# Kernel optimization log

Measured on AMD Instinct MI355X. Metric: run time of the kernel, lower is better.

## Reference

```python
import jax, jax.numpy as jnp
import numpy as np

B, R, C, H, NB, NH, V = 1, 24, 128, 256, 2, 8, 32
DFF = 4 * H


def _ln(x, g, b):
    m = x.mean(-1, keepdims=True)
    v = x.var(-1, keepdims=True)
    return (x - m) / jnp.sqrt(v + 1e-5) * g + b


def _attn(x, wq, wk, wv, wo):
    # x: [..., S, H]; full (dense) multi-head self-attention over axis -2
    d = H // NH
    lead = x.shape[:-1]
    q = (x @ wq).reshape(*lead, NH, d)
    k = (x @ wk).reshape(*lead, NH, d)
    v = (x @ wv).reshape(*lead, NH, d)
    s = jnp.einsum('...qhd,...khd->...hqk', q, k) / np.float32(np.sqrt(d))
    p = jax.nn.softmax(s, axis=-1)
    o = jnp.einsum('...hqk,...khd->...qhd', p, v)
    return o.reshape(*lead, H) @ wo


def setup_inputs() -> dict:
    key = jax.random.key(0)
    ks = iter(jax.random.split(key, 40))

    def nrm(shape, s=0.02):
        return jax.random.normal(next(ks), shape, jnp.float32) * s

    # pair matrix: C(R,2) rows, each selecting (summing) two sequences
    pairs = np.array([(i, j) for i in range(R) for j in range(i + 1, R)], np.int64)
    P = pairs.shape[0]  # 276
    pm = np.zeros((P, R), np.float32)
    pm[np.arange(P)[:, None], pairs] = 1.0

    inp = {
        'x': jax.random.randint(next(ks), (B, R, C), 0, V, jnp.int32),
        'pm': jnp.asarray(pm),
        'emb': nrm((V, H), 1.0),
        'ln1_g': jnp.ones((NB, H)), 'ln1_b': jnp.zeros((NB, H)),
        'wq_r': nrm((NB, H, H)), 'wk_r': nrm((NB, H, H)),
        'wv_r': nrm((NB, H, H)), 'wo_r': nrm((NB, H, H)),
        'ln2_g': jnp.ones((NB, H)), 'ln2_b': jnp.zeros((NB, H)),
        'wq_c': nrm((NB, H, H)), 'wk_c': nrm((NB, H, H)),
        'wv_c': nrm((NB, H, H)), 'wo_c': nrm((NB, H, H)),
        'ln3_g': jnp.ones((NB, H)), 'ln3_b': jnp.zeros((NB, H)),
        'fw1': nrm((NB, H, DFF)), 'fb1': jnp.zeros((NB, DFF)),
        'fw2': nrm((NB, DFF, H)), 'fb2': jnp.zeros((NB, H)),
        'pw1': nrm((H, DFF)), 'pb1': jnp.zeros((DFF,)),
        'pw2': nrm((DFF, 1)), 'pb2': jnp.zeros((1,)),
        'uw': nrm((C, 1)), 'ub': jnp.zeros((1,)),
    }
    return inp


def reference(x, pm, emb, ln1_g, ln1_b, wq_r, wk_r, wv_r, wo_r,
              ln2_g, ln2_b, wq_c, wk_c, wv_c, wo_c, ln3_g, ln3_b,
              fw1, fb1, fw2, fb2, pw1, pb1, pw2, pb2, uw, ub):
    h = emb[x]                                   # [B,R,C,H]
    # pair_matrix @ x : pairwise gather-add over the row (sequence) axis
    h = jnp.einsum('pr,brch->bpch', pm, h)       # [B,P,C,H]
    for i in range(NB):
        # row attention: along columns C, independent per pair
        h = h + _attn(_ln(h, ln1_g[i], ln1_b[i]), wq_r[i], wk_r[i], wv_r[i], wo_r[i])
        # column attention: along pairs P, independent per column
        hc = jnp.swapaxes(h, 1, 2)               # [B,C,P,H]
        a = _attn(_ln(hc, ln2_g[i], ln2_b[i]), wq_c[i], wk_c[i], wv_c[i], wo_c[i])
        h = h + jnp.swapaxes(a, 1, 2)
        # feed-forward
        z = _ln(h, ln3_g[i], ln3_b[i])
        h = h + (jax.nn.gelu(z @ fw1[i] + fb1[i], approximate=False) @ fw2[i] + fb2[i])
    y = jax.nn.gelu(h @ pw1 + pb1, approximate=False) @ pw2 + pb2  # [B,P,C,1]
    y = y.squeeze(-1)                            # [B,P,C]
    y = (y @ uw + ub).squeeze(-1)                # [B,P]
    return y
```

## Files before the change

### kernel.cpp

```cpp
#include <hip/hip_runtime.h>
#include <math.h>

#define HH    256
#define NHEAD 8
#define HD    32
#define CC    128
#define RR    24
#define PP    276
#define NBLK  2
#define DFF   1024
#define MTOK  (PP*CC)

typedef float          f32x4  __attribute__((ext_vector_type(4)));
typedef short          bf16x8 __attribute__((ext_vector_type(8)));
typedef unsigned int   u32x2  __attribute__((ext_vector_type(2)));
typedef unsigned short u16;

__device__ __forceinline__ float gelu_f(float x) {
    return 0.5f * x * (1.0f + erff(x * 0.7071067811865476f));
}
__device__ __forceinline__ u16 f2b(float f) {
    unsigned u = __builtin_bit_cast(unsigned, f);
    unsigned r = (u + 0x7fffu + ((u >> 16) & 1u)) >> 16;
    return (u16)r;
}
__device__ __forceinline__ float b2f(u16 b) {
    unsigned u = ((unsigned)b) << 16;
    return __builtin_bit_cast(float, u);
}
__device__ __forceinline__ unsigned cvt_pk_bf16(float lo, float hi) {
    unsigned r;
    asm("v_cvt_pk_bf16_f32 %0, %1, %2" : "=v"(r) : "v"(lo), "v"(hi));
    return r;
}
__device__ __forceinline__ void gload16(const void* g, void* l) {
    __builtin_amdgcn_global_load_lds(
        (const __attribute__((address_space(1))) unsigned int*)g,
        (__attribute__((address_space(3))) unsigned int*)l, 16, 0, 0);
}

__global__ __launch_bounds__(256) void k_embed(
    const int* __restrict__ x, const float* __restrict__ pm,
    const float* __restrict__ emb, float* __restrict__ h) {
    const int p = blockIdx.x, c = blockIdx.y, t = threadIdx.x;
    float acc = 0.f;
    for (int r = 0; r < RR; ++r) {
        float w = pm[p * RR + r];
        if (w != 0.f) {
            int tok = x[r * CC + c];
            acc += w * emb[(size_t)tok * HH + t];
        }
    }
    h[((size_t)p * CC + c) * HH + t] = acc;
}

__global__ __launch_bounds__(256) void k_ln(
    const float* __restrict__ in, u16* __restrict__ out,
    const float* __restrict__ g, const float* __restrict__ b) {
    const int lane = threadIdx.x & 63, wid = threadIdx.x >> 6;
    const float4 gv = *(const float4*)&g[lane * 4];
    const float4 bv = *(const float4*)&b[lane * 4];
    #pragma unroll
    for (int rr = 0; rr < 2; ++rr) {
        const int row = blockIdx.x * 8 + wid * 2 + rr;
        const float4 v = *(const float4*)&in[(size_t)row * HH + lane * 4];
        float s  = v.x + v.y + v.z + v.w;
        float s2 = v.x * v.x + v.y * v.y + v.z * v.z + v.w * v.w;
        #pragma unroll
        for (int off = 32; off; off >>= 1) {
            s  += __shfl_xor(s,  off);
            s2 += __shfl_xor(s2, off);
        }
        const float mean = s * (1.f / HH);
        const float rstd = rsqrtf(s2 * (1.f / HH) - mean * mean + 1e-5f);
        const float o0 = (v.x - mean) * rstd * gv.x + bv.x;
        const float o1 = (v.y - mean) * rstd * gv.y + bv.y;
        const float o2 = (v.z - mean) * rstd * gv.z + bv.z;
        const float o3 = (v.w - mean) * rstd * gv.w + bv.w;
        u32x2 o;
        o.x = cvt_pk_bf16(o0, o1);
        o.y = cvt_pk_bf16(o2, o3);
        *(u32x2*)&out[(size_t)row * HH + lane * 4] = o;
    }
}

__global__ __launch_bounds__(256) void k_cvtT(
    const float* __restrict__ src, u16* __restrict__ dst,
    int R, int Cc, int dstStride, float mul) {
    __shared__ float tile[32][33];
    const size_t so = (size_t)blockIdx.z * R * Cc;
    const size_t dOff = (size_t)blockIdx.z * dstStride;
    const int r0 = blockIdx.x * 32, c0 = blockIdx.y * 32;
    const int tx = threadIdx.x & 31, ty = threadIdx.x >> 5;
    #pragma unroll
    for (int i = 0; i < 4; ++i)
        tile[ty + 8 * i][tx] = src[so + (size_t)(r0 + ty + 8 * i) * Cc + c0 + tx];
    __syncthreads();
    #pragma unroll
    for (int i = 0; i < 4; ++i)
        dst[dOff + (size_t)(c0 + ty + 8 * i) * R + r0 + tx] = f2b(mul * tile[tx][ty + 8 * i]);
}

#define BM 128
#define BN 64
#define BK 32
template<bool BIAS, bool GELU, bool RES, bool OF32, bool OBF16>
__global__ __launch_bounds__(256) void k_mgemm(
    const u16* __restrict__ A,
    const u16* __restrict__ Wt,
    const float* __restrict__ bias,
    float* __restrict__ C,
    u16* __restrict__ Cb,
    int M, int N, int K) {
    __shared__ __align__(16) char smem[36864];
    u16 (*Al)[BM * BK] = (u16(*)[BM * BK])smem;
    u16 (*Bl)[BN * BK] = (u16(*)[BN * BK])(smem + 24576);
    const int tid = threadIdx.x;
    const int wid = tid >> 6, lane = tid & 63;
    const int wr = wid >> 1, wc = wid & 1;
    const int l16 = lane & 15, lh = lane >> 4;

    const int nwg = gridDim.x;
    const int ntx = N >> 6;
    const int swz = (blockIdx.x & 7) * (nwg >> 3) + (blockIdx.x >> 3);
    const int row0 = (swz / ntx) * BM, col0 = (swz % ntx) * BN;

    int rA[2], pA[2];
    #pragma unroll
    for (int i = 0; i < 2; ++i) {
        const int d = tid + i * 256;
        rA[i] = d >> 2;
        pA[i] = (d & 3) ^ ((rA[i] >> 1) & 3);
    }
    const int nB = tid >> 2;
    const int pB = (tid & 3) ^ ((nB >> 1) & 3);
    const int nt = K / BK;

    auto stage = [&](int buf, int kt) {
        #pragma unroll
        for (int i = 0; i < 2; ++i)
            gload16(A + (size_t)(row0 + rA[i]) * K + kt + pA[i] * 8,
                    (char*)&Al[buf][0] + (wid * 64 + i * 256) * 16);
        gload16(Wt + (size_t)(col0 + nB) * K + kt + pB * 8,
                (char*)&Bl[buf][0] + (wid * 64) * 16);
    };

    f32x4 acc[4][2];
    #pragma unroll
    for (int m = 0; m < 4; ++m)
        #pragma unroll
        for (int n = 0; n < 2; ++n) acc[m][n] = (f32x4){0.f, 0.f, 0.f, 0.f};

    stage(0, 0);
    stage(1, BK);
    for (int t = 0; t < nt; ++t) {
        const int cur = t % 3;
        if (t + 1 < nt) asm volatile("s_waitcnt vmcnt(3)" ::: "memory");
        else            asm volatile("s_waitcnt vmcnt(0)" ::: "memory");
        __builtin_amdgcn_s_barrier();
        __builtin_amdgcn_sched_barrier(0);
        if (t + 2 < nt) stage((t + 2) % 3, (t + 2) * BK);
        bf16x8 af[4], bfr[2];
        #pragma unroll
        for (int m = 0; m < 4; ++m) {
            const int r = wr * 64 + m * 16 + l16;
            af[m] = *(const bf16x8*)((const char*)&Al[cur][0]
                     + r * 64 + ((lh ^ ((r >> 1) & 3)) << 4));
        }
        #pragma unroll
        for (int n = 0; n < 2; ++n) {
            const int nn = wc * 32 + n * 16 + l16;
            bfr[n] = *(const bf16x8*)((const char*)&Bl[cur][0]
                     + nn * 64 + ((lh ^ ((nn >> 1) & 3)) << 4));
        }
        asm volatile("s_waitcnt lgkmcnt(0)" ::: "memory");
        __builtin_amdgcn_sched_barrier(0);
        __builtin_amdgcn_s_setprio(1);
        #pragma unroll
        for (int m = 0; m < 4; ++m)
            #pragma unroll
            for (int n = 0; n < 2; ++n)
                acc[m][n] = __builtin_amdgcn_mfma_f32_16x16x32_bf16(
                    bfr[n], af[m], acc[m][n], 0, 0, 0);
        __builtin_amdgcn_s_setprio(0);
    }

    __syncthreads();
    char* Ct = smem;
    const int lh4 = lh * 4;
    #pragma unroll
    for (int m = 0; m < 4; ++m) {
        const int r = wr * 64 + m * 16 + l16;
        #pragma unroll
        for (int n = 0; n < 2; ++n) {
            const int c = wc * 32 + n * 16 + lh4;
            const int bo = (r * BN + c) * 4 ^ ((r & 7) << 4);
            *(f32x4*)(Ct + bo) = acc[m][n];
        }
    }
    __syncthreads();
    #pragma unroll
    for (int i = 0; i < 8; ++i) {
        const int chunk = tid + i * 256;
        const int r = chunk >> 4, c4 = (chunk & 15) * 4;
        const int bo = (r * BN + c4) * 4 ^ ((r & 7) << 4);
        f32x4 v = *(const f32x4*)(Ct + bo);
        const int colg = col0 + c4;
        const size_t off = (size_t)(row0 + r) * N + colg;
        if (BIAS) v += *(const f32x4*)&bias[colg];
        if (GELU) {
            v[0] = gelu_f(v[0]); v[1] = gelu_f(v[1]);
            v[2] = gelu_f(v[2]); v[3] = gelu_f(v[3]);
        }
        if (RES) v += *(const f32x4*)&C[off];
        if (OF32) __builtin_nontemporal_store(v, (f32x4*)&C[off]);
        if (OBF16) {
            u32x2 o;
            o.x = cvt_pk_bf16(v[0], v[1]);
            o.y = cvt_pk_bf16(v[2], v[3]);
            __builtin_nontemporal_store(o, (u32x2*)&Cb[off]);
        }
    }
}

template<int NQT>
__global__ __launch_bounds__(384) void k_fattn(
    const u16* __restrict__ qg, const u16* __restrict__ kg,
    const u16* __restrict__ vg, u16* __restrict__ og,
    int S, int base_mul, int stride, int rowH) {
    const int head = blockIdx.y;
    const int base = blockIdx.x * base_mul;
    const int tid  = threadIdx.x;
    const int w = tid >> 6, lane = tid & 63;
    const int l16 = lane & 15, lh = lane >> 4;

    __shared__ u16 Vt[32 * 296];

    const int nkt = (S + 15) >> 4;
    const int nch = (nkt + 1) >> 1;
    const int KP  = nch * 32;

    unsigned* Vw = (unsigned*)Vt;
    for (int it = tid; it < (KP >> 1) * 4; it += blockDim.x) {
        const int kp = it >> 2, d8 = (it & 3) * 8;
        const int k0 = kp * 2, k1 = k0 + 1;
        uint4 a = make_uint4(0u, 0u, 0u, 0u), b = a;
        if (k0 < S) a = *(const uint4*)(vg + (size_t)(base + k0 * stride) * rowH + head * HD + d8);
        if (k1 < S) b = *(const uint4*)(vg + (size_t)(base + k1 * stride) * rowH + head * HD + d8);
        Vw[(d8 + 0) * 148 + kp] = (a.x & 0xffffu) | (b.x << 16);
        Vw[(d8 + 1) * 148 + kp] = (a.x >> 16)     | (b.x & 0xffff0000u);
        Vw[(d8 + 2) * 148 + kp] = (a.y & 0xffffu) | (b.y << 16);
        Vw[(d8 + 3) * 148 + kp] = (a.y >> 16)     | (b.y & 0xffff0000u);
        Vw[(d8 + 4) * 148 + kp] = (a.z & 0xffffu) | (b.z << 16);
        Vw[(d8 + 5) * 148 + kp] = (a.z >> 16)     | (b.z & 0xffff0000u);
        Vw[(d8 + 6) * 148 + kp] = (a.w & 0xffffu) | (b.w << 16);
        Vw[(d8 + 7) * 148 + kp] = (a.w >> 16)     | (b.w & 0xffff0000u);
    }
    __syncthreads();

    bf16x8 qf[NQT];
    #pragma unroll
    for (int j = 0; j < NQT; ++j) {
        int qi = (w * NQT + j) * 16 + l16;
        int qc = qi < S ? qi : S - 1;
        qf[j] = *(const bf16x8*)(qg + (size_t)(base + qc * stride) * rowH + head * HD + lh * 8);
    }
    f32x4 acc[NQT][2];
    float mM[NQT], lL[NQT];
    #pragma unroll
    for (int j = 0; j < NQT; ++j) {
        acc[j][0] = (f32x4){0.f, 0.f, 0.f, 0.f};
        acc[j][1] = (f32x4){0.f, 0.f, 0.f, 0.f};
        mM[j] = -1e30f; lL[j] = 0.f;
    }

    auto ldK = [&](int kid) -> bf16x8 {
        int kc = kid < S ? kid : S - 1;
        return *(const bf16x8*)(kg + (size_t)(base + kc * stride) * rowH + head * HD + lh * 8);
    };
    auto ldV = [&](int ch, int dm) -> bf16x8 {
        return *(const bf16x8*)(Vt + (dm * 16 + l16) * 296 + ch * 32 + lh * 8);
    };

    bf16x8 kc0 = ldK(l16), kc1 = ldK(16 + l16);
    bf16x8 vc0 = ldV(0, 0), vc1 = ldV(0, 1);
    const int g0 = 2 * (lh & 1);
    const int src0 = l16 + 16 * g0, src1 = src0 + 16;
    const bool hiT = (lh >> 1) & 1;
    const int lh4 = lh * 4;

    for (int ch = 0; ch < nch; ++ch) {
        const int chn = (ch + 1 < nch) ? ch + 1 : ch;
        bf16x8 kn0 = ldK(chn * 32 + l16);
        bf16x8 kn1 = ldK(chn * 32 + 16 + l16);
        bf16x8 vn0 = ldV(chn, 0);
        bf16x8 vn1 = ldV(chn, 1);
        const int kb = ch * 32;
        const bool fullv = (kb + 32 <= S);
        #pragma unroll
        for (int j = 0; j < NQT; ++j) {
            f32x4 s0 = __builtin_amdgcn_mfma_f32_16x16x32_bf16(
                kc0, qf[j], (f32x4){0.f, 0.f, 0.f, 0.f}, 0, 0, 0);
            f32x4 s1 = __builtin_amdgcn_mfma_f32_16x16x32_bf16(
                kc1, qf[j], (f32x4){0.f, 0.f, 0.f, 0.f}, 0, 0, 0);
            if (!fullv) {
                #pragma unroll
                for (int i = 0; i < 4; ++i) {
                    s0[i] = (kb + lh4 + i      < S) ? s0[i] : -1e30f;
                    s1[i] = (kb + 16 + lh4 + i < S) ? s1[i] : -1e30f;
                }
            }
            float mx = fmaxf(fmaxf(fmaxf(s0[0], s0[1]), fmaxf(s0[2], s0[3])),
                             fmaxf(fmaxf(s1[0], s1[1]), fmaxf(s1[2], s1[3])));
            mx = fmaxf(mx, __shfl_xor(mx, 16));
            mx = fmaxf(mx, __shfl_xor(mx, 32));
            const float mn = fmaxf(mM[j], mx);
            const float corr = __expf(mM[j] - mn);
            mM[j] = mn;
            float p0[4], p1[4], ls = 0.f;
            #pragma unroll
            for (int i = 0; i < 4; ++i) {
                p0[i] = __expf(s0[i] - mn); ls += p0[i];
                p1[i] = __expf(s1[i] - mn); ls += p1[i];
            }
            lL[j] = lL[j] * corr + ls;
            acc[j][0] *= corr;
            acc[j][1] *= corr;
            const int w00 = (int)cvt_pk_bf16(p0[0], p0[1]);
            const int w01 = (int)cvt_pk_bf16(p0[2], p0[3]);
            const int w10 = (int)cvt_pk_bf16(p1[0], p1[1]);
            const int w11 = (int)cvt_pk_bf16(p1[2], p1[3]);
            uint4 W;
            { int a = __shfl(w00, src0), b = __shfl(w10, src0); W.x = (unsigned)(hiT ? b : a); }
            { int a = __shfl(w01, src0), b = __shfl(w11, src0); W.y = (unsigned)(hiT ? b : a); }
            { int a = __shfl(w00, src1), b = __shfl(w10, src1); W.z = (unsigned)(hiT ? b : a); }
            { int a = __shfl(w01, src1), b = __shfl(w11, src1); W.w = (unsigned)(hiT ? b : a); }
            const bf16x8 pw = __builtin_bit_cast(bf16x8, W);
            acc[j][0] = __builtin_amdgcn_mfma_f32_16x16x32_bf16(vc0, pw, acc[j][0], 0, 0, 0);
            acc[j][1] = __builtin_amdgcn_mfma_f32_16x16x32_bf16(vc1, pw, acc[j][1], 0, 0, 0);
        }
        kc0 = kn0; kc1 = kn1; vc0 = vn0; vc1 = vn1;
    }

    #pragma unroll
    for (int j = 0; j < NQT; ++j) {
        float lf = lL[j];
        lf += __shfl_xor(lf, 16);
        lf += __shfl_xor(lf, 32);
        const float inv = 1.f / lf;
        const int qi = (w * NQT + j) * 16 + l16;
        if (qi < S) {
            u16* dst = og + (size_t)(base + qi * stride) * HH + head * HD + lh4;
            #pragma unroll
            for (int dm = 0; dm < 2; ++dm) {
                u32x2 o2;
                o2.x = cvt_pk_bf16(acc[j][dm][0] * inv, acc[j][dm][1] * inv);
                o2.y = cvt_pk_bf16(acc[j][dm][2] * inv, acc[j][dm][3] * inv);
                *(u32x2*)(dst + dm * 16) = o2;
            }
        }
    }
}

__global__ __launch_bounds__(256) void k_head1(
    const u16* __restrict__ g, const float* __restrict__ pw2,
    const float* __restrict__ pb2, float* __restrict__ y) {
    const int tok = blockIdx.x, t = threadIdx.x;
    const ushort4 r4 = *(const ushort4*)&g[(size_t)tok * DFF + t * 4];
    const float4  w4 = *(const float4*)&pw2[t * 4];
    float s = b2f(r4.x) * w4.x + b2f(r4.y) * w4.y
            + b2f(r4.z) * w4.z + b2f(r4.w) * w4.w;
    #pragma unroll
    for (int off = 32; off; off >>= 1) s += __shfl_down(s, off);
    __shared__ float sm[4];
    if ((t & 63) == 0) sm[t >> 6] = s;
    __syncthreads();
    if (t == 0) y[tok] = sm[0] + sm[1] + sm[2] + sm[3] + pb2[0];
}

__global__ __launch_bounds__(128) void k_head2(
    const float* __restrict__ y, const float* __restrict__ uw,
    const float* __restrict__ ub, float* __restrict__ out) {
    const int p = blockIdx.x, t = threadIdx.x;
    float s = y[(size_t)p * CC + t] * uw[t];
    #pragma unroll
    for (int off = 32; off; off >>= 1) s += __shfl_down(s, off);
    __shared__ float sm[2];
    if ((t & 63) == 0) sm[t >> 6] = s;
    __syncthreads();
    if (t == 0) out[p] = sm[0] + sm[1] + ub[0];
}

extern "C" void kernel_launch(void* const* d_in, const int* in_sizes, int n_in,
                              void* d_out, int out_size, void* d_ws, size_t ws_size,
                              hipStream_t stream) {
    (void)in_sizes; (void)n_in; (void)out_size; (void)ws_size;
    const int*   x    = (const int*)  d_in[0];
    const float* pm   = (const float*)d_in[1];
    const float* emb  = (const float*)d_in[2];
    const float* ln1g = (const float*)d_in[3];
    const float* ln1b = (const float*)d_in[4];
    const float* wqr  = (const float*)d_in[5];
    const float* wkr  = (const float*)d_in[6];
    const float* wvr  = (const float*)d_in[7];
    const float* wor  = (const float*)d_in[8];
    const float* ln2g = (const float*)d_in[9];
    const float* ln2b = (const float*)d_in[10];
    const float* wqc  = (const float*)d_in[11];
    const float* wkc  = (const float*)d_in[12];
    const float* wvc  = (const float*)d_in[13];
    const float* woc  = (const float*)d_in[14];
    const float* ln3g = (const float*)d_in[15];
    const float* ln3b = (const float*)d_in[16];
    const float* fw1  = (const float*)d_in[17];
    const float* fb1  = (const float*)d_in[18];
    const float* fw2  = (const float*)d_in[19];
    const float* fb2  = (const float*)d_in[20];
    const float* pw1  = (const float*)d_in[21];
    const float* pb1  = (const float*)d_in[22];
    const float* pw2  = (const float*)d_in[23];
    const float* pb2  = (const float*)d_in[24];
    const float* uw   = (const float*)d_in[25];
    const float* ub   = (const float*)d_in[26];
    float* out = (float*)d_out;

    char* wsp = (char*)d_ws;
    float* h   = (float*)wsp;
    u16*   zb  = (u16*)(wsp + 36175872);
    u16*   hb  = zb + (size_t)MTOK * HH;
    u16*   wts = hb + (size_t)MTOK * HH;
    float* yb  = (float*)((char*)wts + 4718592);
    u16*   scratch = (u16*)((char*)yb + 141312);
    u16* qkvb = scratch;
    u16* bigb = scratch;

    u16* wqkvr_t = wts;
    u16* wqkvc_t = wqkvr_t + 2 * 768 * HH;
    u16* wor_t   = wqkvc_t + 2 * 768 * HH;
    u16* woc_t   = wor_t + 2 * HH * HH;
    u16* fw1t    = woc_t + 2 * HH * HH;
    u16* fw2t    = fw1t + 2 * HH * DFF;
    u16* pw1t    = fw2t + 2 * HH * DFF;

    const float qscale = 0.17677669529663687f;
    const int QKVS = 768 * HH;

    k_cvtT<<<dim3(8, 8, 2),  256, 0, stream>>>(wqr, wqkvr_t,            HH, HH, QKVS, qscale);
    k_cvtT<<<dim3(8, 8, 2),  256, 0, stream>>>(wkr, wqkvr_t + 256 * HH, HH, HH, QKVS, 1.f);
    k_cvtT<<<dim3(8, 8, 2),  256, 0, stream>>>(wvr, wqkvr_t + 512 * HH, HH, HH, QKVS, 1.f);
    k_cvtT<<<dim3(8, 8, 2),  256, 0, stream>>>(wqc, wqkvc_t,            HH, HH, QKVS, qscale);
    k_cvtT<<<dim3(8, 8, 2),  256, 0, stream>>>(wkc, wqkvc_t + 256 * HH, HH, HH, QKVS, 1.f);
    k_cvtT<<<dim3(8, 8, 2),  256, 0, stream>>>(wvc, wqkvc_t + 512 * HH, HH, HH, QKVS, 1.f);
    k_cvtT<<<dim3(8, 8, 2),  256, 0, stream>>>(wor, wor_t, HH, HH, HH * HH, 1.f);
    k_cvtT<<<dim3(8, 8, 2),  256, 0, stream>>>(woc, woc_t, HH, HH, HH * HH, 1.f);
    k_cvtT<<<dim3(8, 32, 2), 256, 0, stream>>>(fw1, fw1t, HH, DFF, HH * DFF, 1.f);
    k_cvtT<<<dim3(32, 8, 2), 256, 0, stream>>>(fw2, fw2t, DFF, HH, HH * DFF, 1.f);
    k_cvtT<<<dim3(8, 32, 1), 256, 0, stream>>>(pw1, pw1t, HH, DFF, 0, 1.f);

    const int gQKV = (MTOK / BM) * (768 / BN);
    const int gO   = (MTOK / BM) * (HH  / BN);
    const int gUp  = (MTOK / BM) * (DFF / BN);

    k_embed<<<dim3(PP, CC), 256, 0, stream>>>(x, pm, emb, h);

    for (int i = 0; i < NBLK; ++i) {
        k_ln<<<MTOK / 8, 256, 0, stream>>>(h, zb, ln1g + i * HH, ln1b + i * HH);
        k_mgemm<false,false,false,false,true><<<gQKV, 256, 0, stream>>>(
            zb, wqkvr_t + (size_t)i * QKVS, nullptr, nullptr, qkvb, MTOK, 768, HH);
        k_fattn<2><<<dim3(PP, NHEAD), 256, 0, stream>>>(
            qkvb, qkvb + 256, qkvb + 512, zb, CC, CC, 1, 768);
        k_mgemm<false,false,true,true,false><<<gO, 256, 0, stream>>>(
            zb, wor_t + (size_t)i * HH * HH, nullptr, h, nullptr, MTOK, HH, HH);
        k_ln<<<MTOK / 8, 256, 0, stream>>>(h, zb, ln2g + i * HH, ln2b + i * HH);
        k_mgemm<false,false,false,false,true><<<gQKV, 256, 0, stream>>>(
            zb, wqkvc_t + (size_t)i * QKVS, nullptr, nullptr, qkvb, MTOK, 768, HH);
        k_fattn<3><<<dim3(CC, NHEAD), 384, 0, stream>>>(
            qkvb, qkvb + 256, qkvb + 512, zb, PP, 1, CC, 768);
        k_mgemm<false,false,true,true,false><<<gO, 256, 0, stream>>>(
            zb, woc_t + (size_t)i * HH * HH, nullptr, h, nullptr, MTOK, HH, HH);
        k_ln<<<MTOK / 8, 256, 0, stream>>>(h, zb, ln3g + i * HH, ln3b + i * HH);
        k_mgemm<true,true,false,false,true><<<gUp, 256, 0, stream>>>(
            zb, fw1t + (size_t)i * HH * DFF, fb1 + i * DFF, nullptr, bigb, MTOK, DFF, HH);
        if (i == NBLK - 1)
            k_mgemm<true,false,true,true,true><<<gO, 256, 0, stream>>>(
                bigb, fw2t + (size_t)i * HH * DFF, fb2 + i * HH, h, hb, MTOK, HH, DFF);
        else
            k_mgemm<true,false,true,true,false><<<gO, 256, 0, stream>>>(
                bigb, fw2t + (size_t)i * HH * DFF, fb2 + i * HH, h, nullptr, MTOK, HH, DFF);
    }

    k_mgemm<true,true,false,false,true><<<gUp, 256, 0, stream>>>(
        hb, pw1t, pb1, nullptr, bigb, MTOK, DFF, HH);
    k_head1<<<MTOK, 256, 0, stream>>>(bigb, pw2, pb2, yb);
    k_head2<<<PP, 128, 0, stream>>>(yb, uw, ub, out);
}
```

Before: 694.0 us.

## Fuse row-attention QKV projection into the flash attention kernel

Adds a row-attention kernel that computes the per-head Q, K and V projections with MFMA directly from the layer-normed activations. It keeps them in shared memory and then runs the online-softmax attention, replacing the separate QKV GEMM and its round trip through global memory. Each (pair, head) block now reloads the whole 128x256 activation tile and its weight slices, so activations are read eight times, once per head. The output goes to the qkv buffer, which then feeds the output projection.

```diff
diff --git a/kernel.cpp b/kernel.cpp
--- a/kernel.cpp
+++ b/kernel.cpp
@@ -223,6 +223,145 @@
     }
 }
 
+__global__ __launch_bounds__(256) void k_fattn_row(
+    const u16* __restrict__ zb, const u16* __restrict__ wt,
+    u16* __restrict__ og) {
+    const int p = blockIdx.x, head = blockIdx.y;
+    const int base = p * CC;
+    const int tid = threadIdx.x;
+    const int w = tid >> 6, lane = tid & 63;
+    const int l16 = lane & 15, lh = lane >> 4;
+    const int lh4 = lh * 4;
+
+    __shared__ u16 Qt[CC * 40];
+    __shared__ u16 Kt[CC * 40];
+    __shared__ u16 Vt[32 * 296];
+
+    const u16* wq = wt + (size_t)(      head * HD) * HH;
+    const u16* wk = wt + (size_t)(256 + head * HD) * HH;
+    const u16* wv = wt + (size_t)(512 + head * HD) * HH;
+    #pragma unroll
+    for (int tt = 0; tt < 2; ++tt) {
+        const int t = w * 2 + tt;
+        f32x4 q0 = (f32x4){0.f,0.f,0.f,0.f}, q1 = q0, k0 = q0, k1 = q0, v0 = q0, v1 = q0;
+        #pragma unroll
+        for (int kk = 0; kk < 8; ++kk) {
+            const int ko = kk * 32 + lh * 8;
+            const bf16x8 z  = *(const bf16x8*)(zb + (size_t)(base + t * 16 + l16) * HH + ko);
+            const bf16x8 fq0 = *(const bf16x8*)(wq + (size_t)(l16)      * HH + ko);
+            const bf16x8 fq1 = *(const bf16x8*)(wq + (size_t)(16 + l16) * HH + ko);
+            const bf16x8 fk0 = *(const bf16x8*)(wk + (size_t)(l16)      * HH + ko);
+            const bf16x8 fk1 = *(const bf16x8*)(wk + (size_t)(16 + l16) * HH + ko);
+            const bf16x8 fv0 = *(const bf16x8*)(wv + (size_t)(l16)      * HH + ko);
+            const bf16x8 fv1 = *(const bf16x8*)(wv + (size_t)(16 + l16) * HH + ko);
+            q0 = __builtin_amdgcn_mfma_f32_16x16x32_bf16(z, fq0, q0, 0, 0, 0);
+            q1 = __builtin_amdgcn_mfma_f32_16x16x32_bf16(z, fq1, q1, 0, 0, 0);
+            k0 = __builtin_amdgcn_mfma_f32_16x16x32_bf16(z, fk0, k0, 0, 0, 0);
+            k1 = __builtin_amdgcn_mfma_f32_16x16x32_bf16(z, fk1, k1, 0, 0, 0);
+            v0 = __builtin_amdgcn_mfma_f32_16x16x32_bf16(fv0, z, v0, 0, 0, 0);
+            v1 = __builtin_amdgcn_mfma_f32_16x16x32_bf16(fv1, z, v1, 0, 0, 0);
+        }
+        #pragma unroll
+        for (int i = 0; i < 4; ++i) {
+            const int tok = t * 16 + lh4 + i;
+            Qt[tok * 40 + l16]      = f2b(q0[i]);
+            Qt[tok * 40 + 16 + l16] = f2b(q1[i]);
+            Kt[tok * 40 + l16]      = f2b(k0[i]);
+            Kt[tok * 40 + 16 + l16] = f2b(k1[i]);
+            Vt[(lh4 + i) * 296 + t * 16 + l16]      = f2b(v0[i]);
+            Vt[(16 + lh4 + i) * 296 + t * 16 + l16] = f2b(v1[i]);
+        }
+    }
+    __syncthreads();
+
+    bf16x8 qf[2];
+    #pragma unroll
+    for (int j = 0; j < 2; ++j) {
+        const int qi = (w * 2 + j) * 16 + l16;
+        qf[j] = *(const bf16x8*)(Qt + qi * 40 + lh * 8);
+    }
+    f32x4 acc[2][2];
+    float mM[2], lL[2];
+    #pragma unroll
+    for (int j = 0; j < 2; ++j) {
+        acc[j][0] = (f32x4){0.f,0.f,0.f,0.f};
+        acc[j][1] = (f32x4){0.f,0.f,0.f,0.f};
+        mM[j] = -1e30f; lL[j] = 0.f;
+    }
+    auto ldK = [&](int kid) -> bf16x8 {
+        return *(const bf16x8*)(Kt + kid * 40 + lh * 8);
+    };
+    auto ldV = [&](int ch, int dm) -> bf16x8 {
+        return *(const bf16x8*)(Vt + (dm * 16 + l16) * 296 + ch * 32 + lh * 8);
+    };
+    bf16x8 kc0 = ldK(l16), kc1 = ldK(16 + l16);
+    bf16x8 vc0 = ldV(0, 0), vc1 = ldV(0, 1);
+    const int g0 = 2 * (lh & 1);
+    const int src0 = l16 + 16 * g0, src1 = src0 + 16;
+    const bool hiT = (lh >> 1) & 1;
+
+    for (int ch = 0; ch < 4; ++ch) {
+        const int chn = (ch + 1 < 4) ? ch + 1 : ch;
+        bf16x8 kn0 = ldK(chn * 32 + l16);
+        bf16x8 kn1 = ldK(chn * 32 + 16 + l16);
+        bf16x8 vn0 = ldV(chn, 0);
+        bf16x8 vn1 = ldV(chn, 1);
+        #pragma unroll
+        for (int j = 0; j < 2; ++j) {
+            f32x4 s0 = __builtin_amdgcn_mfma_f32_16x16x32_bf16(
+                kc0, qf[j], (f32x4){0.f,0.f,0.f,0.f}, 0, 0, 0);
+            f32x4 s1 = __builtin_amdgcn_mfma_f32_16x16x32_bf16(
+                kc1, qf[j], (f32x4){0.f,0.f,0.f,0.f}, 0, 0, 0);
+            float mx = fmaxf(fmaxf(fmaxf(s0[0], s0[1]), fmaxf(s0[2], s0[3])),
+                             fmaxf(fmaxf(s1[0], s1[1]), fmaxf(s1[2], s1[3])));
+            mx = fmaxf(mx, __shfl_xor(mx, 16));
+            mx = fmaxf(mx, __shfl_xor(mx, 32));
+            const float mn = fmaxf(mM[j], mx);
+            const float corr = __expf(mM[j] - mn);
+            mM[j] = mn;
+            float p0[4], p1[4], ls = 0.f;
+            #pragma unroll
+            for (int i = 0; i < 4; ++i) {
+                p0[i] = __expf(s0[i] - mn); ls += p0[i];
+                p1[i] = __expf(s1[i] - mn); ls += p1[i];
+            }
+            lL[j] = lL[j] * corr + ls;
+            acc[j][0] *= corr;
+            acc[j][1] *= corr;
+            const int w00 = (int)cvt_pk_bf16(p0[0], p0[1]);
+            const int w01 = (int)cvt_pk_bf16(p0[2], p0[3]);
+            const int w10 = (int)cvt_pk_bf16(p1[0], p1[1]);
+            const int w11 = (int)cvt_pk_bf16(p1[2], p1[3]);
+            uint4 W;
+            { int a = __shfl(w00, src0), b = __shfl(w10, src0); W.x = (unsigned)(hiT ? b : a); }
+            { int a = __shfl(w01, src0), b = __shfl(w11, src0); W.y = (unsigned)(hiT ? b : a); }
+            { int a = __shfl(w00, src1), b = __shfl(w10, src1); W.z = (unsigned)(hiT ? b : a); }
+            { int a = __shfl(w01, src1), b = __shfl(w11, src1); W.w = (unsigned)(hiT ? b : a); }
+            const bf16x8 pw = __builtin_bit_cast(bf16x8, W);
+            acc[j][0] = __builtin_amdgcn_mfma_f32_16x16x32_bf16(vc0, pw, acc[j][0], 0, 0, 0);
+            acc[j][1] = __builtin_amdgcn_mfma_f32_16x16x32_bf16(vc1, pw, acc[j][1], 0, 0, 0);
+        }
+        kc0 = kn0; kc1 = kn1; vc0 = vn0; vc1 = vn1;
+    }
+
+    #pragma unroll
+    for (int j = 0; j < 2; ++j) {
+        float lf = lL[j];
+        lf += __shfl_xor(lf, 16);
+        lf += __shfl_xor(lf, 32);
+        const float inv = 1.f / lf;
+        const int qi = (w * 2 + j) * 16 + l16;
+        u16* dst = og + (size_t)(base + qi) * HH + head * HD + lh4;
+        #pragma unroll
+        for (int dm = 0; dm < 2; ++dm) {
+            u32x2 o2;
+            o2.x = cvt_pk_bf16(acc[j][dm][0] * inv, acc[j][dm][1] * inv);
+            o2.y = cvt_pk_bf16(acc[j][dm][2] * inv, acc[j][dm][3] * inv);
+            *(u32x2*)(dst + dm * 16) = o2;
+        }
+    }
+}
+
 template<int NQT>
 __global__ __launch_bounds__(384) void k_fattn(
     const u16* __restrict__ qg, const u16* __restrict__ kg,
@@ -269,8 +408,8 @@
     float mM[NQT], lL[NQT];
     #pragma unroll
     for (int j = 0; j < NQT; ++j) {
-        acc[j][0] = (f32x4){0.f, 0.f, 0.f, 0.f};
-        acc[j][1] = (f32x4){0.f, 0.f, 0.f, 0.f};
+        acc[j][0] = (f32x4){0.f,0.f,0.f,0.f};
+        acc[j][1] = (f32x4){0.f,0.f,0.f,0.f};
         mM[j] = -1e30f; lL[j] = 0.f;
     }
 
@@ -300,9 +439,9 @@
         #pragma unroll
         for (int j = 0; j < NQT; ++j) {
             f32x4 s0 = __builtin_amdgcn_mfma_f32_16x16x32_bf16(
-                kc0, qf[j], (f32x4){0.f, 0.f, 0.f, 0.f}, 0, 0, 0);
+                kc0, qf[j], (f32x4){0.f,0.f,0.f,0.f}, 0, 0, 0);
             f32x4 s1 = __builtin_amdgcn_mfma_f32_16x16x32_bf16(
-                kc1, qf[j], (f32x4){0.f, 0.f, 0.f, 0.f}, 0, 0, 0);
+                kc1, qf[j], (f32x4){0.f,0.f,0.f,0.f}, 0, 0, 0);
             if (!fullv) {
                 #pragma unroll
                 for (int i = 0; i < 4; ++i) {
@@ -465,12 +604,10 @@
 
     for (int i = 0; i < NBLK; ++i) {
         k_ln<<<MTOK / 8, 256, 0, stream>>>(h, zb, ln1g + i * HH, ln1b + i * HH);
-        k_mgemm<false,false,false,false,true><<<gQKV, 256, 0, stream>>>(
-            zb, wqkvr_t + (size_t)i * QKVS, nullptr, nullptr, qkvb, MTOK, 768, HH);
-        k_fattn<2><<<dim3(PP, NHEAD), 256, 0, stream>>>(
-            qkvb, qkvb + 256, qkvb + 512, zb, CC, CC, 1, 768);
+        k_fattn_row<<<dim3(PP, NHEAD), 256, 0, stream>>>(
+            zb, wqkvr_t + (size_t)i * QKVS, qkvb);
         k_mgemm<false,false,true,true,false><<<gO, 256, 0, stream>>>(
-            zb, wor_t + (size_t)i * HH * HH, nullptr, h, nullptr, MTOK, HH, HH);
+            qkvb, wor_t + (size_t)i * HH * HH, nullptr, h, nullptr, MTOK, HH, HH);
         k_ln<<<MTOK / 8, 256, 0, stream>>>(h, zb, ln2g + i * HH, ln2b + i * HH);
         k_mgemm<false,false,false,false,true><<<gQKV, 256, 0, stream>>>(
             zb, wqkvc_t + (size_t)i * QKVS, nullptr, nullptr, qkvb, MTOK, 768, HH);
```

After: 819.6 us. 1.18x slower.
